# Optimization experiments

Measured on AMD Instinct MI355X. Metric: run time of the kernel, lower is better.

The kernel has to match this reference:

```python
import jax, jax.numpy as jnp
import numpy as np

TAU = 2.0
VTH = 1.0
H = 8
EPS = 1e-5
SG_ALPHA = 4.0  # spikingjelly surrogate.Sigmoid default alpha


@jax.custom_vjp
def spike(x):
    return (x >= 0.0).astype(x.dtype)

def _spike_fwd(x):
    return (x >= 0.0).astype(x.dtype), x

def _spike_bwd(x, g):
    sg = jax.nn.sigmoid(SG_ALPHA * x)
    return (g * SG_ALPHA * sg * (1.0 - sg),)

spike.defvjp(_spike_fwd, _spike_bwd)


def lif(x, tau=TAU, v_th=VTH):
    # Multi-step LIF, decay_input=True, hard reset to 0, detach_reset=True.
    # x: (T, ...) -> binary spikes (T, ...)
    def step(v, xt):
        v = v + (xt - v) / tau           # charge
        s = spike(v - v_th)              # fire (heaviside w/ surrogate grad)
        v = v * (1.0 - jax.lax.stop_gradient(s))  # hard reset, detached
        return v, s
    v0 = jnp.zeros_like(x[0])
    _, s = jax.lax.scan(step, v0, x)
    return s


def layernorm(y, g, b):
    m = jnp.mean(y, axis=-1, keepdims=True)
    v = jnp.var(y, axis=-1, keepdims=True)
    return (y - m) * jax.lax.rsqrt(v + EPS) * g + b


def setup_inputs() -> dict:
    key = jax.random.key(0)
    T, B, N, D = 4, 32, 197, 512
    Dh = 2048  # int(dim * mlp_ratio)
    ks = jax.random.split(key, 10)
    s = 1.0 / np.sqrt(D)
    sh = 1.0 / np.sqrt(Dh)
    return {
        "x": jax.random.normal(ks[0], (T, B, N, D), dtype=jnp.float32),
        "ln1_g": jnp.ones((D,), jnp.float32),
        "ln1_b": jnp.zeros((D,), jnp.float32),
        "wq": jax.random.normal(ks[1], (D, D), jnp.float32) * s,
        "wk": jax.random.normal(ks[2], (D, D), jnp.float32) * s,
        "wv": jax.random.normal(ks[3], (D, D), jnp.float32) * s,
        "proj_w": jax.random.normal(ks[4], (D, D), jnp.float32) * s,
        "proj_b": jnp.zeros((D,), jnp.float32),
        "ln2_g": jnp.ones((D,), jnp.float32),
        "ln2_b": jnp.zeros((D,), jnp.float32),
        "fc1_w": jax.random.normal(ks[5], (Dh, D), jnp.float32) * s,
        "fc1_b": jnp.zeros((Dh,), jnp.float32),
        "fc2_w": jax.random.normal(ks[6], (D, Dh), jnp.float32) * sh,
        "fc2_b": jnp.zeros((D,), jnp.float32),
    }


def reference(x, ln1_g, ln1_b, wq, wk, wv, proj_w, proj_b,
              ln2_g, ln2_b, fc1_w, fc1_b, fc2_w, fc2_b):
    T, B, N, D = x.shape
    hd = D // H
    scale = hd ** -0.5

    # --- attention branch (pre-norm) ---
    res = x
    y = layernorm(x, ln1_g, ln1_b)
    q = lif(y @ wq.T)                      # (T,B,N,D) binary spikes
    k = lif(y @ wk.T)
    v = lif(y @ wv.T)
    qs = q.reshape(T, B, N, H, hd).transpose(0, 1, 3, 2, 4)  # (T,B,H,N,hd)
    ks = k.reshape(T, B, N, H, hd).transpose(0, 1, 3, 2, 4)
    vs = v.reshape(T, B, N, H, hd).transpose(0, 1, 3, 2, 4)
    attn = jnp.einsum('tbhnd,tbhmd->tbhnm', qs, ks) * scale  # no softmax
    out = jnp.einsum('tbhnm,tbhmd->tbhnd', attn, vs)
    out = out.transpose(0, 1, 3, 2, 4).reshape(T, B, N, D)
    out = lif(out @ proj_w.T + proj_b)
    x = res + out

    # --- spiking MLP branch (pre-norm) ---
    res = x
    y = layernorm(x, ln2_g, ln2_b)
    h = lif(y @ fc1_w.T + fc1_b)
    m = lif(h @ fc2_w.T + fc2_b)
    return res + m
```

## Files before the change

### kernel.cpp

```cpp
#include <hip/hip_runtime.h>
#include <stdint.h>
#include <math.h>

#define T_STEPS 4
#define BB 32
#define NN 197
#define DD 512
#define DH 2048
#define RR (T_STEPS*BB*NN)
#define RPT (BB*NN)
#define LCAP 131072u

typedef unsigned short ushort_t;
typedef unsigned char u8;
typedef __attribute__((ext_vector_type(8))) short bf16x8;
typedef __attribute__((ext_vector_type(4))) float f32x4;

__device__ __forceinline__ float bf2f(ushort_t h) {
    return __uint_as_float(((uint32_t)h) << 16);
}
__device__ __forceinline__ ushort_t f2bf(float f) {
    uint32_t u = __float_as_uint(f);
    uint32_t r = (u + 0x7fffu + ((u >> 16) & 1u)) >> 16;
    return (ushort_t)r;
}
__device__ __forceinline__ f32x4 mfma_bf16(bf16x8 a, bf16x8 b, f32x4 c) {
    return __builtin_amdgcn_mfma_f32_16x16x32_bf16(a, b, c, 0, 0, 0);
}
__device__ __forceinline__ void gll16(const void* gptr, void* lptr) {
    __builtin_amdgcn_global_load_lds(
        (const __attribute__((address_space(1))) uint32_t*)(uintptr_t)gptr,
        (__attribute__((address_space(3))) uint32_t*)(uintptr_t)lptr,
        16, 0, 0);
}
__device__ __forceinline__ double wred(double x) {
#pragma unroll
    for (int o = 32; o; o >>= 1) x += __shfl_xor(x, o, 64);
    return x;
}

__global__ void zero_kernel(uint32_t* p) {
    if (threadIdx.x < 8) p[threadIdx.x] = 0;
}

__global__ __launch_bounds__(256) void wsplit2(const float* __restrict__ w,
    ushort_t* __restrict__ w0, ushort_t* __restrict__ w1, int n) {
    int i = blockIdx.x * 256 + threadIdx.x;
    if (i >= n) return;
    float v = w[i];
    ushort_t h0 = f2bf(v);
    w0[i] = h0;
    w1[i] = f2bf(v - bf2f(h0));
}
__global__ __launch_bounds__(256) void wsplit3(const float* __restrict__ w,
    ushort_t* __restrict__ w0, ushort_t* __restrict__ w1,
    ushort_t* __restrict__ w2, int n) {
    int i = blockIdx.x * 256 + threadIdx.x;
    if (i >= n) return;
    float v = w[i];
    ushort_t h0 = f2bf(v);  float r1 = v - bf2f(h0);
    ushort_t h1 = f2bf(r1); float r2 = r1 - bf2f(h1);
    w0[i] = h0; w1[i] = h1; w2[i] = f2bf(r2);
}

template<int HAS_SP>
__global__ __launch_bounds__(64) void ln_split(
    const float* __restrict__ xin, const u8* __restrict__ spp,
    const float* __restrict__ gw, const float* __restrict__ bw,
    ushort_t* __restrict__ y0, ushort_t* __restrict__ y1)
{
    int id = blockIdx.x;
    int t = id / RPT, rem = id % RPT;
    size_t rp = (size_t)rem * 4 + t;
    int lane = threadIdx.x;

    const float* xp = xin + (size_t)id * DD + (size_t)lane * 8;
    float4 a = *(const float4*)xp;
    float4 bq = *(const float4*)(xp + 4);
    double v[8] = {a.x, a.y, a.z, a.w, bq.x, bq.y, bq.z, bq.w};
    if (HAS_SP) {
        const u8* sp8 = spp + rp * DD + (size_t)lane * 8;
#pragma unroll
        for (int i = 0; i < 8; ++i) v[i] += (double)sp8[i];
    }

    double s = 0.0;
#pragma unroll
    for (int i = 0; i < 8; ++i) s += v[i];
    s = wred(s);
    double m = s * (1.0 / 512.0);
    double d[8], ss = 0.0;
#pragma unroll
    for (int i = 0; i < 8; ++i) { d[i] = v[i] - m; ss += d[i] * d[i]; }
    ss = wred(ss);
    double rstd = 1.0 / sqrt(ss * (1.0 / 512.0) + 1e-5);

    float4 g1 = *(const float4*)(gw + lane * 8);
    float4 g2 = *(const float4*)(gw + lane * 8 + 4);
    float4 b1 = *(const float4*)(bw + lane * 8);
    float4 b2 = *(const float4*)(bw + lane * 8 + 4);
    double gg[8] = {g1.x, g1.y, g1.z, g1.w, g2.x, g2.y, g2.z, g2.w};
    double bb[8] = {b1.x, b1.y, b1.z, b1.w, b2.x, b2.y, b2.z, b2.w};

    bf16x8 o0, o1;
#pragma unroll
    for (int i = 0; i < 8; ++i) {
        float y = (float)(d[i] * rstd * gg[i] + bb[i]);
        ushort_t h0 = f2bf(y);
        o0[i] = (short)h0;
        o1[i] = (short)f2bf(y - bf2f(h0));
    }
    *(bf16x8*)(y0 + rp * DD + lane * 8) = o0;
    *(bf16x8*)(y1 + rp * DD + lane * 8) = o1;
}

template<int NSA, int NSB, int AU8, int EPI>
__global__ __launch_bounds__(256) void gemm128(
    const ushort_t* __restrict__ A0p, const ushort_t* __restrict__ A1p,
    const u8* __restrict__ A8p,
    const ushort_t* __restrict__ B0p, const ushort_t* __restrict__ B1p,
    const ushort_t* __restrict__ B2p,
    const float* __restrict__ biasp, int N, int K, float delta,
    u8* __restrict__ spout, float* __restrict__ fout,
    const float* __restrict__ xres, const u8* __restrict__ spres,
    uint32_t* __restrict__ cnt, uint32_t* __restrict__ list)
{
    __shared__ short lds[(NSA + NSB) * 8192];

    int tid = threadIdx.x, lane = tid & 63, wave = tid >> 6;
    int quad = lane >> 4, r16 = lane & 15;
    int n0 = blockIdx.x * 128, m0 = blockIdx.y * 128;
    int wm = (wave & 1) * 64, wn = (wave >> 1) * 64;

    const ushort_t* Aps[2] = {A0p, A1p};
    const ushort_t* Bps[3] = {B0p, B1p, B2p};

    f32x4 acc[4][4];
#pragma unroll
    for (int rt = 0; rt < 4; ++rt)
#pragma unroll
        for (int ct = 0; ct < 4; ++ct) acc[rt][ct] = (f32x4){0.f,0.f,0.f,0.f};

    for (int k0 = 0; k0 < K; k0 += 64) {
        __syncthreads();
        if (AU8) {
#pragma unroll
            for (int i = 0; i < 2; ++i) {
                int g = i * 256 + tid;
                int row = g >> 2, kc = (g & 3) * 16;
                const u8* src = A8p + (size_t)(m0 + row) * K + k0 + kc;
                uint4 raw = *(const uint4*)src;
                uint32_t wsr[4] = {raw.x, raw.y, raw.z, raw.w};
                short tmp[16];
#pragma unroll
                for (int j = 0; j < 4; ++j)
#pragma unroll
                    for (int bp = 0; bp < 4; ++bp)
                        tmp[j*4+bp] = ((wsr[j] >> (8*bp)) & 0xFFu) ? (short)0x3F80 : (short)0;
                *(bf16x8*)&lds[row * 64 + kc]     = *(bf16x8*)&tmp[0];
                *(bf16x8*)&lds[row * 64 + kc + 8] = *(bf16x8*)&tmp[8];
            }
        } else {
#pragma unroll
            for (int p = 0; p < NSA; ++p)
#pragma unroll
                for (int i = 0; i < 4; ++i) {
                    int c = i * 4 + wave;
                    int row = c * 8 + (lane >> 3);
                    int kc = (lane & 7) * 8;
                    gll16(Aps[p] + (size_t)(m0 + row) * K + k0 + kc,
                          &lds[p * 8192 + c * 512]);
                }
        }
#pragma unroll
        for (int q = 0; q < NSB; ++q)
#pragma unroll
            for (int i = 0; i < 4; ++i) {
                int c = i * 4 + wave;
                int row = c * 8 + (lane >> 3);
                int kc = (lane & 7) * 8;
                gll16(Bps[q] + (size_t)(n0 + row) * K + k0 + kc,
                      &lds[(NSA + q) * 8192 + c * 512]);
            }
        __syncthreads();

#pragma unroll
        for (int sub = 0; sub < 2; ++sub) {
            const int ko = sub * 32 + quad * 8;
            bf16x8 af[4][2], bfv[4][3];
#pragma unroll
            for (int rt = 0; rt < 4; ++rt)
#pragma unroll
                for (int p = 0; p < NSA; ++p)
                    af[rt][p] = *(const bf16x8*)&lds[p * 8192 + (wm + rt*16 + r16) * 64 + ko];
#pragma unroll
            for (int ct = 0; ct < 4; ++ct)
#pragma unroll
                for (int q = 0; q < NSB; ++q)
                    bfv[ct][q] = *(const bf16x8*)&lds[(NSA + q) * 8192 + (wn + ct*16 + r16) * 64 + ko];
#pragma unroll
            for (int rt = 0; rt < 4; ++rt)
#pragma unroll
                for (int ct = 0; ct < 4; ++ct) {
                    f32x4 a = acc[rt][ct];
                    if (NSA == 2)             a = mfma_bf16(af[rt][1], bfv[ct][1], a);
                    if (NSA == 2)             a = mfma_bf16(af[rt][1], bfv[ct][0], a);
                    if (NSB == 3)             a = mfma_bf16(af[rt][0], bfv[ct][2], a);
                    a = mfma_bf16(af[rt][0], bfv[ct][1], a);
                    a = mfma_bf16(af[rt][0], bfv[ct][0], a);
                    acc[rt][ct] = a;
                }
        }
    }

#pragma unroll
    for (int rt = 0; rt < 4; ++rt) {
        int rbase = m0 + wm + rt * 16 + quad * 4;
        int bn = rbase >> 2;
#pragma unroll
        for (int ct = 0; ct < 4; ++ct) {
            int col = n0 + wn + ct * 16 + r16;
            float bv = biasp ? biasp[col] : 0.0f;
            float v = 0.f;
            bool nearf = false;
#pragma unroll
            for (int t = 0; t < 4; ++t) {
                float p = acc[rt][ct][t] + bv;
                v = v + (p - v) * 0.5f;
                nearf |= (fabsf(v - 1.0f) < delta);
                int s = (v >= 1.0f);
                if (EPI == 0) {
                    spout[(size_t)(rbase + t) * N + col] = (u8)s;
                } else {
                    int b = bn / NN, n = bn % NN;
                    size_t oi = (((size_t)t * BB + b) * NN + n) * DD + col;
                    fout[oi] = (float)((double)xres[oi]
                             + (double)spres[(size_t)(rbase + t) * DD + col]
                             + (double)s);
                }
                if (s) v = 0.f;
            }
            if (nearf) {
                uint32_t idx = atomicAdd(cnt, 1u);
                if (idx < LCAP) list[idx] = (uint32_t)bn * (uint32_t)N + (uint32_t)col;
            }
        }
    }
}

template<int ASRC>
__global__ __launch_bounds__(256) void refine_spike(
    const uint32_t* __restrict__ cnt, const uint32_t* __restrict__ list,
    const float* __restrict__ xin, const u8* __restrict__ spres,
    const ushort_t* __restrict__ Ah, const ushort_t* __restrict__ Al,
    const float* __restrict__ lng, const float* __restrict__ lnb,
    const float* __restrict__ W, const float* __restrict__ biasp,
    int N, u8* __restrict__ spout)
{
    int lane = threadIdx.x & 63;
    int wid = (blockIdx.x * 256 + threadIdx.x) >> 6;
    int nw = (gridDim.x * 256) >> 6;
    uint32_t nsus = *cnt; if (nsus > LCAP) nsus = LCAP;
    for (uint32_t i = wid; i < nsus; i += nw) {
        uint32_t id = list[i];
        int col = (int)(id % (uint32_t)N);
        int bn  = (int)(id / (uint32_t)N);
        double p[4];
#pragma unroll
        for (int t = 0; t < 4; ++t) {
            size_t rp = (size_t)bn * 4 + t;
            double dot = 0.0;
            if (ASRC == 0) {
                const float* xr = xin + ((size_t)t * RPT + bn) * DD;
                const u8* sr = spres ? (spres + rp * DD) : (const u8*)nullptr;
                double xv[8], s = 0.0;
#pragma unroll
                for (int j = 0; j < 8; ++j) {
                    int k = j * 64 + lane;
                    double val = (double)xr[k];
                    if (spres) val += (double)sr[k];
                    xv[j] = val; s += val;
                }
                s = wred(s);
                double m = s * (1.0 / 512.0), ss = 0.0;
#pragma unroll
                for (int j = 0; j < 8; ++j) { double d = xv[j] - m; ss += d * d; }
                ss = wred(ss);
                double rstd = 1.0 / sqrt(ss * (1.0 / 512.0) + 1e-5);
#pragma unroll
                for (int j = 0; j < 8; ++j) {
                    int k = j * 64 + lane;
                    double y = (xv[j] - m) * rstd * (double)lng[k] + (double)lnb[k];
                    dot += y * (double)W[(size_t)col * DD + k];
                }
            } else {
#pragma unroll
                for (int j = 0; j < 8; ++j) {
                    int k = j * 64 + lane;
                    double av = (double)bf2f(Ah[rp * DD + k]) + (double)bf2f(Al[rp * DD + k]);
                    dot += av * (double)W[(size_t)col * DD + k];
                }
            }
            dot = wred(dot);
            p[t] = dot + (biasp ? (double)biasp[col] : 0.0);
        }
        if (lane == 0) {
            double v = 0.0;
#pragma unroll
            for (int t = 0; t < 4; ++t) {
                v = v + (p[t] - v) * 0.5;
                int s = (v >= 1.0);
                spout[(size_t)(bn * 4 + t) * N + col] = (u8)s;
                if (s) v = 0.0;
            }
        }
    }
}

__global__ __launch_bounds__(256) void refine_out(
    const uint32_t* __restrict__ cnt, const uint32_t* __restrict__ list,
    const u8* __restrict__ hsp, const float* __restrict__ W,
    const float* __restrict__ biasp,
    const float* __restrict__ xin, const u8* __restrict__ spres,
    float* __restrict__ fout)
{
    int lane = threadIdx.x & 63;
    int wid = (blockIdx.x * 256 + threadIdx.x) >> 6;
    int nw = (gridDim.x * 256) >> 6;
    uint32_t nsus = *cnt; if (nsus > LCAP) nsus = LCAP;
    for (uint32_t i = wid; i < nsus; i += nw) {
        uint32_t id = list[i];
        int col = (int)(id % (uint32_t)DD);
        int bn  = (int)(id / (uint32_t)DD);
        double p[4];
#pragma unroll
        for (int t = 0; t < 4; ++t) {
            size_t rp = (size_t)bn * 4 + t;
            double dot = 0.0;
#pragma unroll
            for (int j = 0; j < 32; ++j) {
                int k = j * 64 + lane;
                dot += (double)hsp[rp * DH + k] * (double)W[(size_t)col * DH + k];
            }
            dot = wred(dot);
            p[t] = dot + (double)biasp[col];
        }
        if (lane == 0) {
            int b = bn / NN, n = bn % NN;
            double v = 0.0;
#pragma unroll
            for (int t = 0; t < 4; ++t) {
                v = v + (p[t] - v) * 0.5;
                int s = (v >= 1.0);
                size_t oi = (((size_t)t * BB + b) * NN + n) * DD + col;
                fout[oi] = (float)((double)xin[oi]
                         + (double)spres[(size_t)(bn * 4 + t) * DD + col]
                         + (double)s);
                if (s) v = 0.0;
            }
        }
    }
}

__global__ __launch_bounds__(256) void attn_kernel(
    const u8* __restrict__ qs, const u8* __restrict__ ks,
    const u8* __restrict__ vs,
    ushort_t* __restrict__ Ah, ushort_t* __restrict__ Al)
{
    __shared__ __align__(16) short sm[29696];
    short* Kt = sm;
    short* Vt = sm + 14848;
    short* MT = sm + 25088;
    short* Qsm = sm;

    int bid = blockIdx.x;
    int t = bid >> 8;
    int b = (bid >> 3) & 31;
    int h = bid & 7;
    size_t base = ((size_t)(b * NN) * 4 + t) * DD + (size_t)h * 64;
    const size_t rstride = (size_t)4 * DD;

    int tid = threadIdx.x;
    int lane = tid & 63, wave = tid >> 6;
    int quad = lane >> 4, r16 = lane & 15;

    for (int i = tid; i < 224 * 16; i += 256) {
        int n = i >> 4;
        int d4 = (i & 15) * 4;
        short kv[4] = {0,0,0,0}, vv[4] = {0,0,0,0};
        if (n < NN) {
            uchar4 kq = *(const uchar4*)(ks + base + (size_t)n * rstride + d4);
            uchar4 vq = *(const uchar4*)(vs + base + (size_t)n * rstride + d4);
            kv[0] = kq.x ? (short)0x3F80 : 0; kv[1] = kq.y ? (short)0x3F80 : 0;
            kv[2] = kq.z ? (short)0x3F80 : 0; kv[3] = kq.w ? (short)0x3F80 : 0;
            vv[0] = vq.x ? (short)0x3F80 : 0; vv[1] = vq.y ? (short)0x3F80 : 0;
            vv[2] = vq.z ? (short)0x3F80 : 0; vv[3] = vq.w ? (short)0x3F80 : 0;
        }
#pragma unroll
        for (int j = 0; j < 4; ++j) {
            Kt[(d4 + j) * 232 + n] = kv[j];
            Vt[(d4 + j) * 232 + n] = vv[j];
        }
    }
    __syncthreads();

    f32x4 accM[4];
#pragma unroll
    for (int c = 0; c < 4; ++c) accM[c] = (f32x4){0.f,0.f,0.f,0.f};
#pragma unroll
    for (int kc = 0; kc < 7; ++kc) {
        int ko = kc * 32 + quad * 8;
        bf16x8 a = *(const bf16x8*)&Kt[(wave * 16 + r16) * 232 + ko];
#pragma unroll
        for (int c = 0; c < 4; ++c) {
            bf16x8 bfr = *(const bf16x8*)&Vt[(c * 16 + r16) * 232 + ko];
            accM[c] = mfma_bf16(a, bfr, accM[c]);
        }
    }
    __syncthreads();

#pragma unroll
    for (int c = 0; c < 4; ++c)
#pragma unroll
        for (int reg = 0; reg < 4; ++reg) {
            int d1 = wave * 16 + quad * 4 + reg;
            int d2 = c * 16 + r16;
            MT[d2 * 72 + d1] = (short)(__float_as_uint(accM[c][reg]) >> 16);
        }
    for (int i = tid; i < 224 * 16; i += 256) {
        int n = i >> 4;
        int d4 = (i & 15) * 4;
        short qv[4] = {0,0,0,0};
        if (n < NN) {
            uchar4 qq = *(const uchar4*)(qs + base + (size_t)n * rstride + d4);
            qv[0] = qq.x ? (short)0x3F80 : 0; qv[1] = qq.y ? (short)0x3F80 : 0;
            qv[2] = qq.z ? (short)0x3F80 : 0; qv[3] = qq.w ? (short)0x3F80 : 0;
        }
        Qsm[n * 72 + d4 + 0] = qv[0];
        Qsm[n * 72 + d4 + 1] = qv[1];
        Qsm[n * 72 + d4 + 2] = qv[2];
        Qsm[n * 72 + d4 + 3] = qv[3];
    }
    __syncthreads();

    for (int rt = wave; rt < 14; rt += 4) {
        f32x4 acc[4];
#pragma unroll
        for (int c = 0; c < 4; ++c) acc[c] = (f32x4){0.f,0.f,0.f,0.f};
#pragma unroll
        for (int kc = 0; kc < 2; ++kc) {
            int ko = kc * 32 + quad * 8;
            bf16x8 a = *(const bf16x8*)&Qsm[(rt * 16 + r16) * 72 + ko];
#pragma unroll
            for (int c = 0; c < 4; ++c) {
                bf16x8 bfr = *(const bf16x8*)&MT[(c * 16 + r16) * 72 + ko];
                acc[c] = mfma_bf16(a, bfr, acc[c]);
            }
        }
#pragma unroll
        for (int c = 0; c < 4; ++c)
#pragma unroll
            for (int reg = 0; reg < 4; ++reg) {
                int n = rt * 16 + quad * 4 + reg;
                if (n < NN) {
                    float val = acc[c][reg] * 0.125f;
                    ushort_t hv = f2bf(val);
                    float lo = val - bf2f(hv);
                    size_t off = base + (size_t)n * rstride + c * 16 + r16;
                    Ah[off] = hv;
                    Al[off] = f2bf(lo);
                }
            }
    }
}

extern "C" void kernel_launch(void* const* d_in, const int* in_sizes, int n_in,
                              void* d_out, int out_size, void* d_ws, size_t ws_size,
                              hipStream_t stream)
{
    const float* x      = (const float*)d_in[0];
    const float* ln1_g  = (const float*)d_in[1];
    const float* ln1_b  = (const float*)d_in[2];
    const float* wq     = (const float*)d_in[3];
    const float* wk     = (const float*)d_in[4];
    const float* wv     = (const float*)d_in[5];
    const float* proj_w = (const float*)d_in[6];
    const float* proj_b = (const float*)d_in[7];
    const float* ln2_g  = (const float*)d_in[8];
    const float* ln2_b  = (const float*)d_in[9];
    const float* fc1_w  = (const float*)d_in[10];
    const float* fc1_b  = (const float*)d_in[11];
    const float* fc2_w  = (const float*)d_in[12];
    const float* fc2_b  = (const float*)d_in[13];
    float* outp = (float*)d_out;

    const size_t P1 = (size_t)RR * DD;
    char* wsb = (char*)d_ws;
    ushort_t* A0  = (ushort_t*)(wsb + 0);
    ushort_t* A1  = (ushort_t*)(wsb + P1 * 2);
    u8*       qs  = (u8*)(wsb + P1 * 4);
    u8*       ksp = (u8*)(wsb + P1 * 5);
    u8*       vsp = (u8*)(wsb + P1 * 6);
    u8*       sp  = (u8*)(wsb + P1 * 7);
    ushort_t* Ah  = (ushort_t*)(wsb + P1 * 8);
    ushort_t* Al  = (ushort_t*)(wsb + P1 * 10);
    u8*       hsp = (u8*)(wsb + P1 * 8);
    char*     wpl = wsb + P1 * 12;
    ushort_t* wq0 = (ushort_t*)(wpl);
    ushort_t* wq1 = wq0 + (size_t)DD * DD;
    ushort_t* wk0 = wq1 + (size_t)DD * DD;
    ushort_t* wk1 = wk0 + (size_t)DD * DD;
    ushort_t* wv0 = wk1 + (size_t)DD * DD;
    ushort_t* wv1 = wv0 + (size_t)DD * DD;
    ushort_t* wp0 = wv1 + (size_t)DD * DD;
    ushort_t* wp1 = wp0 + (size_t)DD * DD;
    ushort_t* wp2 = wp1 + (size_t)DD * DD;
    ushort_t* f10 = wp2 + (size_t)DD * DD;
    ushort_t* f11 = f10 + (size_t)DH * DD;
    ushort_t* f20 = f11 + (size_t)DH * DD;
    ushort_t* f21 = f20 + (size_t)DD * DH;
    uint32_t* cnt  = (uint32_t*)((char*)(f21 + (size_t)DD * DH) + 0);
    uint32_t* list = (uint32_t*)((char*)cnt + 256);

    zero_kernel<<<1, 64, 0, stream>>>(cnt);

    wsplit2<<<(DD*DD+255)/256, 256, 0, stream>>>(wq, wq0, wq1, DD*DD);
    wsplit2<<<(DD*DD+255)/256, 256, 0, stream>>>(wk, wk0, wk1, DD*DD);
    wsplit2<<<(DD*DD+255)/256, 256, 0, stream>>>(wv, wv0, wv1, DD*DD);
    wsplit3<<<(DD*DD+255)/256, 256, 0, stream>>>(proj_w, wp0, wp1, wp2, DD*DD);
    wsplit2<<<(DH*DD+255)/256, 256, 0, stream>>>(fc1_w, f10, f11, DH*DD);
    wsplit2<<<(DD*DH+255)/256, 256, 0, stream>>>(fc2_w, f20, f21, DD*DH);

    ln_split<0><<<RR, 64, 0, stream>>>(x, nullptr, ln1_g, ln1_b, A0, A1);

    dim3 g8(4, RR/128), g32(DH/128, RR/128);
    gemm128<2,2,0,0><<<g8, 256, 0, stream>>>(A0, A1, nullptr, wq0, wq1, nullptr,
        nullptr, DD, DD, 3e-4f, qs, nullptr, nullptr, nullptr, cnt+0, list+0*LCAP);
    gemm128<2,2,0,0><<<g8, 256, 0, stream>>>(A0, A1, nullptr, wk0, wk1, nullptr,
        nullptr, DD, DD, 3e-4f, ksp, nullptr, nullptr, nullptr, cnt+1, list+1*LCAP);
    gemm128<2,2,0,0><<<g8, 256, 0, stream>>>(A0, A1, nullptr, wv0, wv1, nullptr,
        nullptr, DD, DD, 3e-4f, vsp, nullptr, nullptr, nullptr, cnt+2, list+2*LCAP);
    refine_spike<0><<<128, 256, 0, stream>>>(cnt+0, list+0*LCAP, x, nullptr,
        nullptr, nullptr, ln1_g, ln1_b, wq, nullptr, DD, qs);
    refine_spike<0><<<128, 256, 0, stream>>>(cnt+1, list+1*LCAP, x, nullptr,
        nullptr, nullptr, ln1_g, ln1_b, wk, nullptr, DD, ksp);
    refine_spike<0><<<128, 256, 0, stream>>>(cnt+2, list+2*LCAP, x, nullptr,
        nullptr, nullptr, ln1_g, ln1_b, wv, nullptr, DD, vsp);

    attn_kernel<<<T_STEPS * BB * 8, 256, 0, stream>>>(qs, ksp, vsp, Ah, Al);

    gemm128<2,3,0,0><<<g8, 256, 0, stream>>>(Ah, Al, nullptr, wp0, wp1, wp2,
        proj_b, DD, DD, 1e-3f, sp, nullptr, nullptr, nullptr, cnt+3, list+3*LCAP);
    refine_spike<1><<<128, 256, 0, stream>>>(cnt+3, list+3*LCAP, nullptr, nullptr,
        Ah, Al, nullptr, nullptr, proj_w, proj_b, DD, sp);

    ln_split<1><<<RR, 64, 0, stream>>>(x, sp, ln2_g, ln2_b, A0, A1);

    gemm128<2,2,0,0><<<g32, 256, 0, stream>>>(A0, A1, nullptr, f10, f11, nullptr,
        fc1_b, DH, DD, 3e-4f, hsp, nullptr, nullptr, nullptr, cnt+4, list+4*LCAP);
    refine_spike<0><<<128, 256, 0, stream>>>(cnt+4, list+4*LCAP, x, sp,
        nullptr, nullptr, ln2_g, ln2_b, fc1_w, fc1_b, DH, hsp);

    gemm128<1,2,1,2><<<g8, 256, 0, stream>>>(nullptr, nullptr, hsp, f20, f21, nullptr,
        fc2_b, DD, DH, 3e-4f, nullptr, outp, x, sp, cnt+5, list+5*LCAP);
    refine_out<<<128, 256, 0, stream>>>(cnt+5, list+5*LCAP, hsp, fc2_w, fc2_b,
        x, sp, outp);
}
```

Measured before the change: 1.074 ms.

## Swizzle LDS tiles, fuse QKV GEMM, and split refine kernels

```diff
diff --git a/kernel.cpp b/kernel.cpp
--- a/kernel.cpp
+++ b/kernel.cpp
@@ -38,41 +38,48 @@
     for (int o = 32; o; o >>= 1) x += __shfl_xor(x, o, 64);
     return x;
 }
+__device__ __forceinline__ int swzk(int k, int row) {
+    return (k & ~63) | ((k & 63) ^ ((row & 7) << 3));
+}
 
 __global__ void zero_kernel(uint32_t* p) {
     if (threadIdx.x < 8) p[threadIdx.x] = 0;
 }
 
 __global__ __launch_bounds__(256) void wsplit2(const float* __restrict__ w,
-    ushort_t* __restrict__ w0, ushort_t* __restrict__ w1, int n) {
+    ushort_t* __restrict__ w0, ushort_t* __restrict__ w1, int n, int K) {
     int i = blockIdx.x * 256 + threadIdx.x;
     if (i >= n) return;
+    int row = i / K;
+    int so = (i & ~63) | ((i & 63) ^ ((row & 7) << 3));
     float v = w[i];
     ushort_t h0 = f2bf(v);
-    w0[i] = h0;
-    w1[i] = f2bf(v - bf2f(h0));
+    w0[so] = h0;
+    w1[so] = f2bf(v - bf2f(h0));
 }
 __global__ __launch_bounds__(256) void wsplit3(const float* __restrict__ w,
     ushort_t* __restrict__ w0, ushort_t* __restrict__ w1,
-    ushort_t* __restrict__ w2, int n) {
+    ushort_t* __restrict__ w2, int n, int K) {
     int i = blockIdx.x * 256 + threadIdx.x;
     if (i >= n) return;
+    int row = i / K;
+    int so = (i & ~63) | ((i & 63) ^ ((row & 7) << 3));
     float v = w[i];
     ushort_t h0 = f2bf(v);  float r1 = v - bf2f(h0);
     ushort_t h1 = f2bf(r1); float r2 = r1 - bf2f(h1);
-    w0[i] = h0; w1[i] = h1; w2[i] = f2bf(r2);
+    w0[so] = h0; w1[so] = h1; w2[so] = f2bf(r2);
 }
 
 template<int HAS_SP>
-__global__ __launch_bounds__(64) void ln_split(
+__global__ __launch_bounds__(256) void ln_split(
     const float* __restrict__ xin, const u8* __restrict__ spp,
     const float* __restrict__ gw, const float* __restrict__ bw,
     ushort_t* __restrict__ y0, ushort_t* __restrict__ y1)
 {
-    int id = blockIdx.x;
+    int wave = threadIdx.x >> 6, lane = threadIdx.x & 63;
+    int id = blockIdx.x * 4 + wave;
     int t = id / RPT, rem = id % RPT;
     size_t rp = (size_t)rem * 4 + t;
-    int lane = threadIdx.x;
 
     const float* xp = xin + (size_t)id * DD + (size_t)lane * 8;
     float4 a = *(const float4*)xp;
@@ -110,18 +117,20 @@
         o0[i] = (short)h0;
         o1[i] = (short)f2bf(y - bf2f(h0));
     }
-    *(bf16x8*)(y0 + rp * DD + lane * 8) = o0;
-    *(bf16x8*)(y1 + rp * DD + lane * 8) = o1;
-}
-
-template<int NSA, int NSB, int AU8, int EPI>
+    size_t off = rp * DD + swzk(lane * 8, (int)rp);
+    *(bf16x8*)(y0 + off) = o0;
+    *(bf16x8*)(y1 + off) = o1;
+}
+
+template<int NSA, int NSB, int AU8, int EPI, int NMAT>
 __global__ __launch_bounds__(256) void gemm128(
     const ushort_t* __restrict__ A0p, const ushort_t* __restrict__ A1p,
     const u8* __restrict__ A8p,
     const ushort_t* __restrict__ B0p, const ushort_t* __restrict__ B1p,
     const ushort_t* __restrict__ B2p,
     const float* __restrict__ biasp, int N, int K, float delta,
-    u8* __restrict__ spout, float* __restrict__ fout,
+    u8* __restrict__ s0, u8* __restrict__ s1, u8* __restrict__ s2,
+    float* __restrict__ fout,
     const float* __restrict__ xres, const u8* __restrict__ spres,
     uint32_t* __restrict__ cnt, uint32_t* __restrict__ list)
 {
@@ -148,6 +157,7 @@
             for (int i = 0; i < 2; ++i) {
                 int g = i * 256 + tid;
                 int row = g >> 2, kc = (g & 3) * 16;
+                int sw = (row & 7) << 3;
                 const u8* src = A8p + (size_t)(m0 + row) * K + k0 + kc;
                 uint4 raw = *(const uint4*)src;
                 uint32_t wsr[4] = {raw.x, raw.y, raw.z, raw.w};
@@ -157,8 +167,8 @@
 #pragma unroll
                     for (int bp = 0; bp < 4; ++bp)
                         tmp[j*4+bp] = ((wsr[j] >> (8*bp)) & 0xFFu) ? (short)0x3F80 : (short)0;
-                *(bf16x8*)&lds[row * 64 + kc]     = *(bf16x8*)&tmp[0];
-                *(bf16x8*)&lds[row * 64 + kc + 8] = *(bf16x8*)&tmp[8];
+                *(bf16x8*)&lds[row * 64 + (kc ^ sw)]       = *(bf16x8*)&tmp[0];
+                *(bf16x8*)&lds[row * 64 + ((kc + 8) ^ sw)] = *(bf16x8*)&tmp[8];
             }
         } else {
 #pragma unroll
@@ -189,23 +199,27 @@
             const int ko = sub * 32 + quad * 8;
             bf16x8 af[4][2], bfv[4][3];
 #pragma unroll
-            for (int rt = 0; rt < 4; ++rt)
+            for (int rt = 0; rt < 4; ++rt) {
+                int r = wm + rt * 16 + r16;
 #pragma unroll
                 for (int p = 0; p < NSA; ++p)
-                    af[rt][p] = *(const bf16x8*)&lds[p * 8192 + (wm + rt*16 + r16) * 64 + ko];
-#pragma unroll
-            for (int ct = 0; ct < 4; ++ct)
+                    af[rt][p] = *(const bf16x8*)&lds[p * 8192 + r * 64 + (ko ^ ((r & 7) << 3))];
+            }
+#pragma unroll
+            for (int ct = 0; ct < 4; ++ct) {
+                int r = wn + ct * 16 + r16;
 #pragma unroll
                 for (int q = 0; q < NSB; ++q)
-                    bfv[ct][q] = *(const bf16x8*)&lds[(NSA + q) * 8192 + (wn + ct*16 + r16) * 64 + ko];
+                    bfv[ct][q] = *(const bf16x8*)&lds[(NSA + q) * 8192 + r * 64 + (ko ^ ((r & 7) << 3))];
+            }
 #pragma unroll
             for (int rt = 0; rt < 4; ++rt)
 #pragma unroll
                 for (int ct = 0; ct < 4; ++ct) {
                     f32x4 a = acc[rt][ct];
-                    if (NSA == 2)             a = mfma_bf16(af[rt][1], bfv[ct][1], a);
+                    if (NSB == 3)             a = mfma_bf16(af[rt][0], bfv[ct][2], a);
+                    if (NSA == 2 && NSB == 3) a = mfma_bf16(af[rt][1], bfv[ct][1], a);
                     if (NSA == 2)             a = mfma_bf16(af[rt][1], bfv[ct][0], a);
-                    if (NSB == 3)             a = mfma_bf16(af[rt][0], bfv[ct][2], a);
                     a = mfma_bf16(af[rt][0], bfv[ct][1], a);
                     a = mfma_bf16(af[rt][0], bfv[ct][0], a);
                     acc[rt][ct] = a;
@@ -230,7 +244,13 @@
                 nearf |= (fabsf(v - 1.0f) < delta);
                 int s = (v >= 1.0f);
                 if (EPI == 0) {
-                    spout[(size_t)(rbase + t) * N + col] = (u8)s;
+                    if (NMAT == 3) {
+                        int mat = col >> 9, cc = col & 511;
+                        u8* sp = (mat == 0) ? s0 : ((mat == 1) ? s1 : s2);
+                        sp[(size_t)(rbase + t) * 512 + cc] = (u8)s;
+                    } else {
+                        s0[(size_t)(rbase + t) * N + col] = (u8)s;
+                    }
                 } else {
                     int b = bn / NN, n = bn % NN;
                     size_t oi = (((size_t)t * BB + b) * NN + n) * DD + col;
@@ -248,11 +268,78 @@
     }
 }
 
-template<int ASRC>
-__global__ __launch_bounds__(256) void refine_spike(
+__device__ __forceinline__ void ln_recompute_row(
+    const float* __restrict__ xr, const u8* __restrict__ sr, int lane,
+    const float* __restrict__ lng, const float* __restrict__ lnb, double* yv)
+{
+    double xv[8], s = 0.0;
+#pragma unroll
+    for (int j = 0; j < 8; ++j) {
+        int k = j * 64 + lane;
+        double val = (double)xr[k];
+        if (sr) val += (double)sr[k];
+        xv[j] = val; s += val;
+    }
+    s = wred(s);
+    double m = s * (1.0 / 512.0), ss = 0.0;
+#pragma unroll
+    for (int j = 0; j < 8; ++j) { double d = xv[j] - m; ss += d * d; }
+    ss = wred(ss);
+    double rstd = 1.0 / sqrt(ss * (1.0 / 512.0) + 1e-5);
+#pragma unroll
+    for (int j = 0; j < 8; ++j) {
+        int k = j * 64 + lane;
+        yv[j] = (xv[j] - m) * rstd * (double)lng[k] + (double)lnb[k];
+    }
+}
+
+__global__ __launch_bounds__(256) void refine_qkv(
     const uint32_t* __restrict__ cnt, const uint32_t* __restrict__ list,
-    const float* __restrict__ xin, const u8* __restrict__ spres,
-    const ushort_t* __restrict__ Ah, const ushort_t* __restrict__ Al,
+    const float* __restrict__ x,
+    const float* __restrict__ lng, const float* __restrict__ lnb,
+    const float* __restrict__ wq, const float* __restrict__ wk,
+    const float* __restrict__ wv,
+    u8* __restrict__ qs, u8* __restrict__ ks, u8* __restrict__ vs)
+{
+    int lane = threadIdx.x & 63;
+    int wid = (blockIdx.x * 256 + threadIdx.x) >> 6;
+    int nw = (gridDim.x * 256) >> 6;
+    uint32_t nsus = *cnt; if (nsus > LCAP) nsus = LCAP;
+    for (uint32_t i = wid; i < nsus; i += nw) {
+        uint32_t id = list[i];
+        int col1536 = (int)(id % 1536u);
+        int bn = (int)(id / 1536u);
+        int mat = col1536 >> 9, col = col1536 & 511;
+        const float* W = (mat == 0) ? wq : ((mat == 1) ? wk : wv);
+        u8* spout = (mat == 0) ? qs : ((mat == 1) ? ks : vs);
+        double p[4];
+#pragma unroll
+        for (int t = 0; t < 4; ++t) {
+            const float* xr = x + ((size_t)t * RPT + bn) * DD;
+            double yv[8];
+            ln_recompute_row(xr, nullptr, lane, lng, lnb, yv);
+            double dot = 0.0;
+#pragma unroll
+            for (int j = 0; j < 8; ++j)
+                dot += yv[j] * (double)W[(size_t)col * DD + j * 64 + lane];
+            p[t] = wred(dot);
+        }
+        if (lane == 0) {
+            double v = 0.0;
+#pragma unroll
+            for (int t = 0; t < 4; ++t) {
+                v = v + (p[t] - v) * 0.5;
+                int s = (v >= 1.0);
+                spout[(size_t)(bn * 4 + t) * 512 + col] = (u8)s;
+                if (s) v = 0.0;
+            }
+        }
+    }
+}
+
+__global__ __launch_bounds__(256) void refine_ln(
+    const uint32_t* __restrict__ cnt, const uint32_t* __restrict__ list,
+    const float* __restrict__ x, const u8* __restrict__ spres,
     const float* __restrict__ lng, const float* __restrict__ lnb,
     const float* __restrict__ W, const float* __restrict__ biasp,
     int N, u8* __restrict__ spout)
@@ -269,40 +356,15 @@
 #pragma unroll
         for (int t = 0; t < 4; ++t) {
             size_t rp = (size_t)bn * 4 + t;
+            const float* xr = x + ((size_t)t * RPT + bn) * DD;
+            double yv[8];
+            ln_recompute_row(xr, spres + rp * DD, lane, lng, lnb, yv);
             double dot = 0.0;
-            if (ASRC == 0) {
-                const float* xr = xin + ((size_t)t * RPT + bn) * DD;
-                const u8* sr = spres ? (spres + rp * DD) : (const u8*)nullptr;
-                double xv[8], s = 0.0;
-#pragma unroll
-                for (int j = 0; j < 8; ++j) {
-                    int k = j * 64 + lane;
-                    double val = (double)xr[k];
-                    if (spres) val += (double)sr[k];
-                    xv[j] = val; s += val;
-                }
-                s = wred(s);
-                double m = s * (1.0 / 512.0), ss = 0.0;
-#pragma unroll
-                for (int j = 0; j < 8; ++j) { double d = xv[j] - m; ss += d * d; }
-                ss = wred(ss);
-                double rstd = 1.0 / sqrt(ss * (1.0 / 512.0) + 1e-5);
-#pragma unroll
-                for (int j = 0; j < 8; ++j) {
-                    int k = j * 64 + lane;
-                    double y = (xv[j] - m) * rstd * (double)lng[k] + (double)lnb[k];
-                    dot += y * (double)W[(size_t)col * DD + k];
-                }
-            } else {
-#pragma unroll
-                for (int j = 0; j < 8; ++j) {
-                    int k = j * 64 + lane;
-                    double av = (double)bf2f(Ah[rp * DD + k]) + (double)bf2f(Al[rp * DD + k]);
-                    dot += av * (double)W[(size_t)col * DD + k];
-                }
-            }
+#pragma unroll
+            for (int j = 0; j < 8; ++j)
+                dot += yv[j] * (double)W[(size_t)col * DD + j * 64 + lane];
             dot = wred(dot);
-            p[t] = dot + (biasp ? (double)biasp[col] : 0.0);
+            p[t] = dot + (double)biasp[col];
         }
         if (lane == 0) {
             double v = 0.0;
@@ -311,6 +373,48 @@
                 v = v + (p[t] - v) * 0.5;
                 int s = (v >= 1.0);
                 spout[(size_t)(bn * 4 + t) * N + col] = (u8)s;
+                if (s) v = 0.0;
+            }
+        }
+    }
+}
+
+__global__ __launch_bounds__(256) void refine_proj(
+    const uint32_t* __restrict__ cnt, const uint32_t* __restrict__ list,
+    const ushort_t* __restrict__ Ah, const ushort_t* __restrict__ Al,
+    const float* __restrict__ W, const float* __restrict__ biasp,
+    u8* __restrict__ spout)
+{
+    int lane = threadIdx.x & 63;
+    int wid = (blockIdx.x * 256 + threadIdx.x) >> 6;
+    int nw = (gridDim.x * 256) >> 6;
+    uint32_t nsus = *cnt; if (nsus > LCAP) nsus = LCAP;
+    for (uint32_t i = wid; i < nsus; i += nw) {
+        uint32_t id = list[i];
+        int col = (int)(id % (uint32_t)DD);
+        int bn  = (int)(id / (uint32_t)DD);
+        double p[4];
+#pragma unroll
+        for (int t = 0; t < 4; ++t) {
+            size_t rp = (size_t)bn * 4 + t;
+            int sw = ((int)rp & 7) << 3;
+            double dot = 0.0;
+#pragma unroll
+            for (int j = 0; j < 8; ++j) {
+                size_t addr = rp * DD + j * 64 + (lane ^ sw);
+                double a = (double)bf2f(Ah[addr]) + (double)bf2f(Al[addr]);
+                dot += a * (double)W[(size_t)col * DD + j * 64 + lane];
+            }
+            dot = wred(dot);
+            p[t] = dot + (double)biasp[col];
+        }
+        if (lane == 0) {
+            double v = 0.0;
+#pragma unroll
+            for (int t = 0; t < 4; ++t) {
+                v = v + (p[t] - v) * 0.5;
+                int s = (v >= 1.0);
+                spout[(size_t)(bn * 4 + t) * DD + col] = (u8)s;
                 if (s) v = 0.0;
             }
         }
@@ -466,7 +570,8 @@
                     float val = acc[c][reg] * 0.125f;
                     ushort_t hv = f2bf(val);
                     float lo = val - bf2f(hv);
-                    size_t off = base + (size_t)n * rstride + c * 16 + r16;
+                    int sw = ((((b + n) & 1) << 2) | t) << 3;
+                    size_t off = base + (size_t)n * rstride + ((c * 16 + r16) ^ sw);
                     Ah[off] = hv;
                     Al[off] = f2bf(lo);
                 }
@@ -496,73 +601,64 @@
 
     const size_t P1 = (size_t)RR * DD;
     char* wsb = (char*)d_ws;
-    ushort_t* A0  = (ushort_t*)(wsb + 0);
-    ushort_t* A1  = (ushort_t*)(wsb + P1 * 2);
-    u8*       qs  = (u8*)(wsb + P1 * 4);
-    u8*       ksp = (u8*)(wsb + P1 * 5);
-    u8*       vsp = (u8*)(wsb + P1 * 6);
-    u8*       sp  = (u8*)(wsb + P1 * 7);
-    ushort_t* Ah  = (ushort_t*)(wsb + P1 * 8);
-    ushort_t* Al  = (ushort_t*)(wsb + P1 * 10);
-    u8*       hsp = (u8*)(wsb + P1 * 8);
-    char*     wpl = wsb + P1 * 12;
-    ushort_t* wq0 = (ushort_t*)(wpl);
-    ushort_t* wq1 = wq0 + (size_t)DD * DD;
-    ushort_t* wk0 = wq1 + (size_t)DD * DD;
-    ushort_t* wk1 = wk0 + (size_t)DD * DD;
-    ushort_t* wv0 = wk1 + (size_t)DD * DD;
-    ushort_t* wv1 = wv0 + (size_t)DD * DD;
-    ushort_t* wp0 = wv1 + (size_t)DD * DD;
-    ushort_t* wp1 = wp0 + (size_t)DD * DD;
-    ushort_t* wp2 = wp1 + (size_t)DD * DD;
-    ushort_t* f10 = wp2 + (size_t)DD * DD;
-    ushort_t* f11 = f10 + (size_t)DH * DD;
-    ushort_t* f20 = f11 + (size_t)DH * DD;
-    ushort_t* f21 = f20 + (size_t)DD * DH;
-    uint32_t* cnt  = (uint32_t*)((char*)(f21 + (size_t)DD * DH) + 0);
-    uint32_t* list = (uint32_t*)((char*)cnt + 256);
+    size_t off = 0;
+    ushort_t* A0  = (ushort_t*)(wsb + off); off += P1 * 2;
+    ushort_t* A1  = (ushort_t*)(wsb + off); off += P1 * 2;
+    u8*       qs  = (u8*)(wsb + off); off += P1;
+    u8*       ksp = (u8*)(wsb + off); off += P1;
+    u8*       vsp = (u8*)(wsb + off); off += P1;
+    u8*       sp  = (u8*)(wsb + off); off += P1;
+    ushort_t* Ah  = (ushort_t*)(wsb + off); off += P1 * 2;
+    ushort_t* Al  = (ushort_t*)(wsb + off); off += P1 * 2;
+    u8*       hsp = (u8*)Ah;
+    ushort_t* wqkv0 = (ushort_t*)(wsb + off); off += (size_t)3 * DD * DD * 2;
+    ushort_t* wqkv1 = (ushort_t*)(wsb + off); off += (size_t)3 * DD * DD * 2;
+    ushort_t* wp0 = (ushort_t*)(wsb + off); off += (size_t)DD * DD * 2;
+    ushort_t* wp1 = (ushort_t*)(wsb + off); off += (size_t)DD * DD * 2;
+    ushort_t* wp2 = (ushort_t*)(wsb + off); off += (size_t)DD * DD * 2;
+    ushort_t* f10 = (ushort_t*)(wsb + off); off += (size_t)DH * DD * 2;
+    ushort_t* f11 = (ushort_t*)(wsb + off); off += (size_t)DH * DD * 2;
+    ushort_t* f20 = (ushort_t*)(wsb + off); off += (size_t)DD * DH * 2;
+    ushort_t* f21 = (ushort_t*)(wsb + off); off += (size_t)DD * DH * 2;
+    uint32_t* cnt  = (uint32_t*)(wsb + off); off += 256;
+    uint32_t* list = (uint32_t*)(wsb + off);
 
     zero_kernel<<<1, 64, 0, stream>>>(cnt);
 
-    wsplit2<<<(DD*DD+255)/256, 256, 0, stream>>>(wq, wq0, wq1, DD*DD);
-    wsplit2<<<(DD*DD+255)/256, 256, 0, stream>>>(wk, wk0, wk1, DD*DD);
-    wsplit2<<<(DD*DD+255)/256, 256, 0, stream>>>(wv, wv0, wv1, DD*DD);
-    wsplit3<<<(DD*DD+255)/256, 256, 0, stream>>>(proj_w, wp0, wp1, wp2, DD*DD);
-    wsplit2<<<(DH*DD+255)/256, 256, 0, stream>>>(fc1_w, f10, f11, DH*DD);
-    wsplit2<<<(DD*DH+255)/256, 256, 0, stream>>>(fc2_w, f20, f21, DD*DH);
-
-    ln_split<0><<<RR, 64, 0, stream>>>(x, nullptr, ln1_g, ln1_b, A0, A1);
-
-    dim3 g8(4, RR/128), g32(DH/128, RR/128);
-    gemm128<2,2,0,0><<<g8, 256, 0, stream>>>(A0, A1, nullptr, wq0, wq1, nullptr,
-        nullptr, DD, DD, 3e-4f, qs, nullptr, nullptr, nullptr, cnt+0, list+0*LCAP);
-    gemm128<2,2,0,0><<<g8, 256, 0, stream>>>(A0, A1, nullptr, wk0, wk1, nullptr,
-        nullptr, DD, DD, 3e-4f, ksp, nullptr, nullptr, nullptr, cnt+1, list+1*LCAP);
-    gemm128<2,2,0,0><<<g8, 256, 0, stream>>>(A0, A1, nullptr, wv0, wv1, nullptr,
-        nullptr, DD, DD, 3e-4f, vsp, nullptr, nullptr, nullptr, cnt+2, list+2*LCAP);
-    refine_spike<0><<<128, 256, 0, stream>>>(cnt+0, list+0*LCAP, x, nullptr,
-        nullptr, nullptr, ln1_g, ln1_b, wq, nullptr, DD, qs);
-    refine_spike<0><<<128, 256, 0, stream>>>(cnt+1, list+1*LCAP, x, nullptr,
-        nullptr, nullptr, ln1_g, ln1_b, wk, nullptr, DD, ksp);
-    refine_spike<0><<<128, 256, 0, stream>>>(cnt+2, list+2*LCAP, x, nullptr,
-        nullptr, nullptr, ln1_g, ln1_b, wv, nullptr, DD, vsp);
+    wsplit2<<<(DD*DD+255)/256, 256, 0, stream>>>(wq, wqkv0, wqkv1, DD*DD, DD);
+    wsplit2<<<(DD*DD+255)/256, 256, 0, stream>>>(wk, wqkv0 + DD*DD, wqkv1 + DD*DD, DD*DD, DD);
+    wsplit2<<<(DD*DD+255)/256, 256, 0, stream>>>(wv, wqkv0 + 2*DD*DD, wqkv1 + 2*DD*DD, DD*DD, DD);
+    wsplit3<<<(DD*DD+255)/256, 256, 0, stream>>>(proj_w, wp0, wp1, wp2, DD*DD, DD);
+    wsplit2<<<(DH*DD+255)/256, 256, 0, stream>>>(fc1_w, f10, f11, DH*DD, DD);
+    wsplit2<<<(DD*DH+255)/256, 256, 0, stream>>>(fc2_w, f20, f21, DD*DH, DH);
+
+    ln_split<0><<<RR/4, 256, 0, stream>>>(x, nullptr, ln1_g, ln1_b, A0, A1);
+
+    gemm128<2,2,0,0,3><<<dim3(12, RR/128), 256, 0, stream>>>(
+        A0, A1, nullptr, wqkv0, wqkv1, nullptr, nullptr, 1536, DD, 3e-4f,
+        qs, ksp, vsp, nullptr, nullptr, nullptr, cnt + 0, list);
+    refine_qkv<<<128, 256, 0, stream>>>(cnt + 0, list, x, ln1_g, ln1_b,
+        wq, wk, wv, qs, ksp, vsp);
 
     attn_kernel<<<T_STEPS * BB * 8, 256, 0, stream>>>(qs, ksp, vsp, Ah, Al);
 
-    gemm128<2,3,0,0><<<g8, 256, 0, stream>>>(Ah, Al, nullptr, wp0, wp1, wp2,
-        proj_b, DD, DD, 1e-3f, sp, nullptr, nullptr, nullptr, cnt+3, list+3*LCAP);
-    refine_spike<1><<<128, 256, 0, stream>>>(cnt+3, list+3*LCAP, nullptr, nullptr,
-        Ah, Al, nullptr, nullptr, proj_w, proj_b, DD, sp);
-
-    ln_split<1><<<RR, 64, 0, stream>>>(x, sp, ln2_g, ln2_b, A0, A1);
-
-    gemm128<2,2,0,0><<<g32, 256, 0, stream>>>(A0, A1, nullptr, f10, f11, nullptr,
-        fc1_b, DH, DD, 3e-4f, hsp, nullptr, nullptr, nullptr, cnt+4, list+4*LCAP);
-    refine_spike<0><<<128, 256, 0, stream>>>(cnt+4, list+4*LCAP, x, sp,
-        nullptr, nullptr, ln2_g, ln2_b, fc1_w, fc1_b, DH, hsp);
-
-    gemm128<1,2,1,2><<<g8, 256, 0, stream>>>(nullptr, nullptr, hsp, f20, f21, nullptr,
-        fc2_b, DD, DH, 3e-4f, nullptr, outp, x, sp, cnt+5, list+5*LCAP);
-    refine_out<<<128, 256, 0, stream>>>(cnt+5, list+5*LCAP, hsp, fc2_w, fc2_b,
-        x, sp, outp);
-}
+    gemm128<2,3,0,0,1><<<dim3(4, RR/128), 256, 0, stream>>>(
+        Ah, Al, nullptr, wp0, wp1, wp2, proj_b, DD, DD, 1e-3f,
+        sp, nullptr, nullptr, nullptr, nullptr, nullptr, cnt + 1, list + LCAP);
+    refine_proj<<<128, 256, 0, stream>>>(cnt + 1, list + LCAP, Ah, Al,
+        proj_w, proj_b, sp);
+
+    ln_split<1><<<RR/4, 256, 0, stream>>>(x, sp, ln2_g, ln2_b, A0, A1);
+
+    gemm128<2,2,0,0,1><<<dim3(16, RR/128), 256, 0, stream>>>(
+        A0, A1, nullptr, f10, f11, nullptr, fc1_b, DH, DD, 3e-4f,
+        hsp, nullptr, nullptr, nullptr, nullptr, nullptr, cnt + 2, list + 2*LCAP);
+    refine_ln<<<128, 256, 0, stream>>>(cnt + 2, list + 2*LCAP, x, sp,
+        ln2_g, ln2_b, fc1_w, fc1_b, DH, hsp);
+
+    gemm128<1,2,1,2,1><<<dim3(4, RR/128), 256, 0, stream>>>(
+        nullptr, nullptr, hsp, f20, f21, nullptr, fc2_b, DD, DH, 3e-4f,
+        nullptr, nullptr, nullptr, outp, x, sp, cnt + 3, list + 3*LCAP);
+    refine_out<<<128, 256, 0, stream>>>(cnt + 3, list + 3*LCAP, hsp,
+        fc2_w, fc2_b, x, sp, outp);
+}
```

New measurement: 873.1 us. -18.7%, faster.
